# Performance work log

Hardware: AMD Instinct MI355X
Metric: run time of the kernel (lower is better)

## Reference

```python
import jax, jax.numpy as jnp
import numpy as np

B, T, I, H = 4096, 128, 32, 64


def _u(key, shape, bound):
    return jax.random.uniform(key, shape, jnp.float32, -bound, bound)


def setup_inputs() -> dict:
    key = jax.random.key(0)
    ks = jax.random.split(key, 14)
    bound = 1.0 / np.sqrt(H)  # torch LSTM/Linear default init scale
    inp = {
        "x": jax.random.normal(ks[0], (B, T, I), jnp.float32),
        "Wih0": _u(ks[1], (4 * H, I), bound),
        "Whh0": _u(ks[2], (4 * H, H), bound),
        "bih0": _u(ks[3], (4 * H,), bound),
        "bhh0": _u(ks[4], (4 * H,), bound),
        "Wih1": _u(ks[5], (4 * H, H), bound),
        "Whh1": _u(ks[6], (4 * H, H), bound),
        "bih1": _u(ks[7], (4 * H,), bound),
        "bhh1": _u(ks[8], (4 * H,), bound),
        "Wc1": _u(ks[9], (32, H), 1.0 / np.sqrt(H)),
        "bc1": _u(ks[10], (32,), 1.0 / np.sqrt(H)),
        "Wc2": _u(ks[11], (1, 32), 1.0 / np.sqrt(32)),
        "bc2": _u(ks[12], (1,), 1.0 / np.sqrt(32)),
    }
    return inp


def lstm_layer(x_tbi, Wih, Whh, bih, bhh):
    """x_tbi: [T, B, in]. Returns (all hidden [T,B,H], final hidden [B,H]).
    PyTorch gate order: i, f, g, o."""
    b = x_tbi.shape[1]
    h0 = jnp.zeros((b, Whh.shape[1]), x_tbi.dtype)
    c0 = jnp.zeros_like(h0)
    # precompute input projections for all timesteps in one big GEMM
    xproj = jnp.einsum('tbi,gi->tbg', x_tbi, Wih) + (bih + bhh)

    def step(carry, xp_t):
        h, c = carry
        gates = xp_t + h @ Whh.T  # [B, 4H]
        i, f, g, o = jnp.split(gates, 4, axis=-1)
        c = jax.nn.sigmoid(f) * c + jax.nn.sigmoid(i) * jnp.tanh(g)
        h = jax.nn.sigmoid(o) * jnp.tanh(c)
        return (h, c), h

    (hT, _), hs = jax.lax.scan(step, (h0, c0), xproj)
    return hs, hT


def reference(x, Wih0, Whh0, bih0, bhh0, Wih1, Whh1, bih1, bhh1, Wc1, bc1, Wc2, bc2):
    x_tbi = jnp.transpose(x, (1, 0, 2))  # [T, B, I]
    hs0, _ = lstm_layer(x_tbi, Wih0, Whh0, bih0, bhh0)
    # dropout between layers is identity in eval mode
    _, hT = lstm_layer(hs0, Wih1, Whh1, bih1, bhh1)  # h_n[-1]: [B, H]
    hidden = jax.nn.relu(hT @ Wc1.T + bc1)  # [B, 32]; classifier dropout = identity (eval)
    out = hidden @ Wc2.T + bc2  # [B, 1]
    return out.squeeze(-1)  # [B]
```

## Files before the change

kernel.cpp:

```cpp
#include <hip/hip_runtime.h>


#define TT 128
#define II 32
#define HH 64

typedef _Float16 half8 __attribute__((ext_vector_type(8)));
typedef float floatx4 __attribute__((ext_vector_type(4)));

#define LOG2E 1.4426950408889634f

__device__ __forceinline__ half8 load_w_frag(const float* __restrict__ W, int n, int K, int k0) {
    const float* p = W + (size_t)n * K + k0;
    float4 a = *(const float4*)p;
    float4 b = *(const float4*)(p + 4);
    half8 h;
    h[0] = (_Float16)a.x; h[1] = (_Float16)a.y; h[2] = (_Float16)a.z; h[3] = (_Float16)a.w;
    h[4] = (_Float16)b.x; h[5] = (_Float16)b.y; h[6] = (_Float16)b.z; h[7] = (_Float16)b.w;
    return h;
}

__device__ __forceinline__ float sig_tanh(float a, float b) {
    float bb = fminf(fmaxf(b, -15.f), 15.f);
    float u  = __builtin_amdgcn_exp2f(bb * (2.0f * LOG2E));
    float v  = __builtin_amdgcn_exp2f(-a * LOG2E);
    float num = u - 1.0f;
    float d1  = u + 1.0f;
    float den = fmaf(v, d1, d1);
    return num * __builtin_amdgcn_rcpf(den);
}

__device__ __forceinline__ float fsig(float x) {
    return __builtin_amdgcn_rcpf(1.0f + __builtin_amdgcn_exp2f(-x * LOG2E));
}

__global__ __launch_bounds__(512, 2) void lstm_fused(
    const float* __restrict__ x,
    const float* __restrict__ Wih0, const float* __restrict__ Whh0,
    const float* __restrict__ bih0, const float* __restrict__ bhh0,
    const float* __restrict__ Wih1, const float* __restrict__ Whh1,
    const float* __restrict__ bih1, const float* __restrict__ bhh1,
    const float* __restrict__ Wc1, const float* __restrict__ bc1,
    const float* __restrict__ Wc2, const float* __restrict__ bc2,
    float* __restrict__ out)
{
    __shared__ __align__(16) _Float16 xs[2][16][40];
    __shared__ __align__(16) _Float16 h0s[2][16][72];
    __shared__ __align__(16) _Float16 h1s[2][16][72];
    __shared__ __align__(16) float h1f[16][68];
    __shared__ float hid[16][32];

    const int tid  = threadIdx.x;
    const int wid  = tid >> 6;
    const int w4   = wid & 3;
    const bool isL0 = (wid < 4);
    const int lane = tid & 63;
    const int q  = lane >> 4;
    const int lr = lane & 15;
    const int b0 = blockIdx.x * 16;

    half8 bx0[4], bh0[4][2];
    half8 bi1[4][2], bh1[4][2];
    float biasv[4];
    if (isL0) {
        #pragma unroll
        for (int g = 0; g < 4; ++g) {
            int n = (w4 + 4 * g) * 16 + lr;
            bx0[g]    = load_w_frag(Wih0, n, 32, q * 8);
            bh0[g][0] = load_w_frag(Whh0, n, 64, q * 8);
            bh0[g][1] = load_w_frag(Whh0, n, 64, 32 + q * 8);
            biasv[g]  = bih0[n] + bhh0[n];
        }
    } else {
        #pragma unroll
        for (int g = 0; g < 4; ++g) {
            int n = (w4 + 4 * g) * 16 + lr;
            bi1[g][0] = load_w_frag(Wih1, n, 64, q * 8);
            bi1[g][1] = load_w_frag(Wih1, n, 64, 32 + q * 8);
            bh1[g][0] = load_w_frag(Whh1, n, 64, q * 8);
            bh1[g][1] = load_w_frag(Whh1, n, 64, 32 + q * 8);
            biasv[g]  = bih1[n] + bhh1[n];
        }
    }

    for (int i = tid; i < 2 * 16 * 72; i += 512) {
        ((_Float16*)h0s)[i] = (_Float16)0.0f;
        ((_Float16*)h1s)[i] = (_Float16)0.0f;
    }

    float cr[4] = {0.f, 0.f, 0.f, 0.f};

    const int xm = (tid >> 4) & 15;
    const int xf = (tid & 15) * 2;
    const float* xrow = x + ((size_t)(b0 + xm) * TT) * II + xf;
    float2 xbuf = {0.f, 0.f};
    if (isL0) {
        float2 x0 = *(const float2*)(xrow);
        xs[0][xm][xf]     = (_Float16)x0.x;
        xs[0][xm][xf + 1] = (_Float16)x0.y;
        if (TT > 1) xbuf = *(const float2*)(xrow + 1 * II);
    }

    for (int k = 0; k <= TT; ++k) {
        __syncthreads();

        const int rd = (k + 1) & 1;
        const int wr = k & 1;
        const bool doL0 = isL0 && (k < TT);
        const bool doL1 = (!isL0) && (k >= 1);
        float hnew[4];
        float2 xnew = xbuf;

        if (doL0) {
            half8 xfrag = *(const half8*)&xs[wr][lr][q * 8];
            half8 h0a   = *(const half8*)&h0s[rd][lr][q * 8];
            half8 h0b   = *(const half8*)&h0s[rd][lr][32 + q * 8];
            if (k + 2 < TT) xnew = *(const float2*)(xrow + (size_t)(k + 2) * II);
            floatx4 a0[4];
            #pragma unroll
            for (int g = 0; g < 4; ++g) {
                floatx4 acc = {biasv[g], biasv[g], biasv[g], biasv[g]};
                acc = __builtin_amdgcn_mfma_f32_16x16x32_f16(xfrag, bx0[g],    acc, 0, 0, 0);
                acc = __builtin_amdgcn_mfma_f32_16x16x32_f16(h0a,   bh0[g][0], acc, 0, 0, 0);
                acc = __builtin_amdgcn_mfma_f32_16x16x32_f16(h0b,   bh0[g][1], acc, 0, 0, 0);
                a0[g] = acc;
            }
            #pragma unroll
            for (int r = 0; r < 4; ++r) {
                float sf = fsig(a0[1][r]);
                float c  = fmaf(sf, cr[r], sig_tanh(a0[0][r], a0[2][r]));
                cr[r] = c;
                hnew[r] = sig_tanh(a0[3][r], c);
            }
        }
        if (doL1) {
            half8 g0a = *(const half8*)&h0s[rd][lr][q * 8];
            half8 g0b = *(const half8*)&h0s[rd][lr][32 + q * 8];
            half8 h1a = *(const half8*)&h1s[rd][lr][q * 8];
            half8 h1b = *(const half8*)&h1s[rd][lr][32 + q * 8];
            floatx4 a1[4];
            #pragma unroll
            for (int g = 0; g < 4; ++g) {
                floatx4 acc = {biasv[g], biasv[g], biasv[g], biasv[g]};
                acc = __builtin_amdgcn_mfma_f32_16x16x32_f16(g0a, bi1[g][0], acc, 0, 0, 0);
                acc = __builtin_amdgcn_mfma_f32_16x16x32_f16(g0b, bi1[g][1], acc, 0, 0, 0);
                acc = __builtin_amdgcn_mfma_f32_16x16x32_f16(h1a, bh1[g][0], acc, 0, 0, 0);
                acc = __builtin_amdgcn_mfma_f32_16x16x32_f16(h1b, bh1[g][1], acc, 0, 0, 0);
                a1[g] = acc;
            }
            #pragma unroll
            for (int r = 0; r < 4; ++r) {
                float sf = fsig(a1[1][r]);
                float c  = fmaf(sf, cr[r], sig_tanh(a1[0][r], a1[2][r]));
                cr[r] = c;
                hnew[r] = sig_tanh(a1[3][r], c);
            }
        }

        if (doL0) {
            #pragma unroll
            for (int r = 0; r < 4; ++r)
                h0s[wr][q * 4 + r][w4 * 16 + lr] = (_Float16)hnew[r];
            if (k + 1 < TT) {
                xs[rd][xm][xf]     = (_Float16)xbuf.x;
                xs[rd][xm][xf + 1] = (_Float16)xbuf.y;
            }
            xbuf = xnew;
        }
        if (doL1) {
            if (k == TT) {
                #pragma unroll
                for (int r = 0; r < 4; ++r)
                    h1f[q * 4 + r][w4 * 16 + lr] = hnew[r];
            } else {
                #pragma unroll
                for (int r = 0; r < 4; ++r)
                    h1s[wr][q * 4 + r][w4 * 16 + lr] = (_Float16)hnew[r];
            }
        }
    }
    __syncthreads();

    if (tid < 256) {
        int m = tid >> 4;
        int u = (tid & 15) * 2;
        float a = bc1[u], b = bc1[u + 1];
        const float* w0 = Wc1 + u * 64;
        const float* w1 = Wc1 + (u + 1) * 64;
        #pragma unroll 8
        for (int kk = 0; kk < 64; ++kk) {
            float hv = h1f[m][kk];
            a += hv * w0[kk];
            b += hv * w1[kk];
        }
        hid[m][u]     = fmaxf(a, 0.f);
        hid[m][u + 1] = fmaxf(b, 0.f);
    }
    __syncthreads();
    if (tid < 16) {
        float o = bc2[0];
        #pragma unroll
        for (int u = 0; u < 32; ++u) o += hid[tid][u] * Wc2[u];
        out[b0 + tid] = o;
    }
}

extern "C" void kernel_launch(void* const* d_in, const int* in_sizes, int n_in,
                              void* d_out, int out_size, void* d_ws, size_t ws_size,
                              hipStream_t stream) {
    (void)in_sizes; (void)n_in; (void)d_ws; (void)ws_size; (void)out_size;
    const float* x    = (const float*)d_in[0];
    const float* Wih0 = (const float*)d_in[1];
    const float* Whh0 = (const float*)d_in[2];
    const float* bih0 = (const float*)d_in[3];
    const float* bhh0 = (const float*)d_in[4];
    const float* Wih1 = (const float*)d_in[5];
    const float* Whh1 = (const float*)d_in[6];
    const float* bih1 = (const float*)d_in[7];
    const float* bhh1 = (const float*)d_in[8];
    const float* Wc1  = (const float*)d_in[9];
    const float* bc1  = (const float*)d_in[10];
    const float* Wc2  = (const float*)d_in[11];
    const float* bc2  = (const float*)d_in[12];
    lstm_fused<<<dim3(256), dim3(512), 0, stream>>>(
        x, Wih0, Whh0, bih0, bhh0, Wih1, Whh1, bih1, bhh1, Wc1, bc1, Wc2, bc2,
        (float*)d_out);
}
```

Baseline: 203.5 us.

## Precompute next-step input projection off critical path and fold bias into activations

After: 255.8 us. 25.7% more time.

```diff
diff --git a/kernel.cpp b/kernel.cpp
--- a/kernel.cpp
+++ b/kernel.cpp
@@ -3,35 +3,22 @@
 
 #define TT 128
 #define II 32
-#define HH 64
 
 typedef _Float16 half8 __attribute__((ext_vector_type(8)));
 typedef float floatx4 __attribute__((ext_vector_type(4)));
 
 #define LOG2E 1.4426950408889634f
 
-__device__ __forceinline__ half8 load_w_frag(const float* __restrict__ W, int n, int K, int k0) {
-    const float* p = W + (size_t)n * K + k0;
-    float4 a = *(const float4*)p;
-    float4 b = *(const float4*)(p + 4);
+__device__ __forceinline__ half8 cvt_frag(float4 a, float4 b) {
     half8 h;
     h[0] = (_Float16)a.x; h[1] = (_Float16)a.y; h[2] = (_Float16)a.z; h[3] = (_Float16)a.w;
     h[4] = (_Float16)b.x; h[5] = (_Float16)b.y; h[6] = (_Float16)b.z; h[7] = (_Float16)b.w;
     return h;
 }
 
-__device__ __forceinline__ float sig_tanh(float a, float b) {
-    float bb = fminf(fmaxf(b, -15.f), 15.f);
-    float u  = __builtin_amdgcn_exp2f(bb * (2.0f * LOG2E));
-    float v  = __builtin_amdgcn_exp2f(-a * LOG2E);
-    float num = u - 1.0f;
-    float d1  = u + 1.0f;
-    float den = fmaf(v, d1, d1);
-    return num * __builtin_amdgcn_rcpf(den);
-}
-
-__device__ __forceinline__ float fsig(float x) {
-    return __builtin_amdgcn_rcpf(1.0f + __builtin_amdgcn_exp2f(-x * LOG2E));
+__device__ __forceinline__ half8 load_w_frag(const float* __restrict__ W, int n, int K, int k0) {
+    const float* p = W + (size_t)n * K + k0;
+    return cvt_frag(*(const float4*)p, *(const float4*)(p + 4));
 }
 
 __global__ __launch_bounds__(512, 2) void lstm_fused(
@@ -44,7 +31,6 @@
     const float* __restrict__ Wc2, const float* __restrict__ bc2,
     float* __restrict__ out)
 {
-    __shared__ __align__(16) _Float16 xs[2][16][40];
     __shared__ __align__(16) _Float16 h0s[2][16][72];
     __shared__ __align__(16) _Float16 h1s[2][16][72];
     __shared__ __align__(16) float h1f[16][68];
@@ -59,9 +45,13 @@
     const int lr = lane & 15;
     const int b0 = blockIdx.x * 16;
 
+    const float nL  = -LOG2E;
+    const float p2L = 2.0f * LOG2E;
+    const float C43 = 30.0f * LOG2E;
+
     half8 bx0[4], bh0[4][2];
     half8 bi1[4][2], bh1[4][2];
-    float biasv[4];
+    float bias[4];
     if (isL0) {
         #pragma unroll
         for (int g = 0; g < 4; ++g) {
@@ -69,7 +59,7 @@
             bx0[g]    = load_w_frag(Wih0, n, 32, q * 8);
             bh0[g][0] = load_w_frag(Whh0, n, 64, q * 8);
             bh0[g][1] = load_w_frag(Whh0, n, 64, 32 + q * 8);
-            biasv[g]  = bih0[n] + bhh0[n];
+            bias[g]   = bih0[n] + bhh0[n];
         }
     } else {
         #pragma unroll
@@ -79,8 +69,24 @@
             bi1[g][1] = load_w_frag(Wih1, n, 64, 32 + q * 8);
             bh1[g][0] = load_w_frag(Whh1, n, 64, q * 8);
             bh1[g][1] = load_w_frag(Whh1, n, 64, 32 + q * 8);
-            biasv[g]  = bih1[n] + bhh1[n];
-        }
+            bias[g]   = bih1[n] + bhh1[n];
+        }
+    }
+    const float nbi = nL * bias[0], nbf = nL * bias[1];
+    const float bg2 = p2L * bias[2], nbo = nL * bias[3];
+
+    const floatx4 zeroq = {0.f, 0.f, 0.f, 0.f};
+
+    const float* xlane = x + (size_t)(b0 + lr) * TT * II + q * 8;
+    float4 xr0, xr1;
+    floatx4 xacc[4];
+    if (isL0) {
+        half8 xf = cvt_frag(*(const float4*)xlane, *(const float4*)(xlane + 4));
+        #pragma unroll
+        for (int g = 0; g < 4; ++g)
+            xacc[g] = __builtin_amdgcn_mfma_f32_16x16x32_f16(xf, bx0[g], zeroq, 0, 0, 0);
+        xr0 = *(const float4*)(xlane + II);
+        xr1 = *(const float4*)(xlane + II + 4);
     }
 
     for (int i = tid; i < 2 * 16 * 72; i += 512) {
@@ -89,17 +95,6 @@
     }
 
     float cr[4] = {0.f, 0.f, 0.f, 0.f};
-
-    const int xm = (tid >> 4) & 15;
-    const int xf = (tid & 15) * 2;
-    const float* xrow = x + ((size_t)(b0 + xm) * TT) * II + xf;
-    float2 xbuf = {0.f, 0.f};
-    if (isL0) {
-        float2 x0 = *(const float2*)(xrow);
-        xs[0][xm][xf]     = (_Float16)x0.x;
-        xs[0][xm][xf + 1] = (_Float16)x0.y;
-        if (TT > 1) xbuf = *(const float2*)(xrow + 1 * II);
-    }
 
     for (int k = 0; k <= TT; ++k) {
         __syncthreads();
@@ -108,29 +103,16 @@
         const int wr = k & 1;
         const bool doL0 = isL0 && (k < TT);
         const bool doL1 = (!isL0) && (k >= 1);
+        floatx4 a[4];
         float hnew[4];
-        float2 xnew = xbuf;
 
         if (doL0) {
-            half8 xfrag = *(const half8*)&xs[wr][lr][q * 8];
-            half8 h0a   = *(const half8*)&h0s[rd][lr][q * 8];
-            half8 h0b   = *(const half8*)&h0s[rd][lr][32 + q * 8];
-            if (k + 2 < TT) xnew = *(const float2*)(xrow + (size_t)(k + 2) * II);
-            floatx4 a0[4];
+            half8 h0a = *(const half8*)&h0s[rd][lr][q * 8];
+            half8 h0b = *(const half8*)&h0s[rd][lr][32 + q * 8];
             #pragma unroll
             for (int g = 0; g < 4; ++g) {
-                floatx4 acc = {biasv[g], biasv[g], biasv[g], biasv[g]};
-                acc = __builtin_amdgcn_mfma_f32_16x16x32_f16(xfrag, bx0[g],    acc, 0, 0, 0);
-                acc = __builtin_amdgcn_mfma_f32_16x16x32_f16(h0a,   bh0[g][0], acc, 0, 0, 0);
-                acc = __builtin_amdgcn_mfma_f32_16x16x32_f16(h0b,   bh0[g][1], acc, 0, 0, 0);
-                a0[g] = acc;
-            }
-            #pragma unroll
-            for (int r = 0; r < 4; ++r) {
-                float sf = fsig(a0[1][r]);
-                float c  = fmaf(sf, cr[r], sig_tanh(a0[0][r], a0[2][r]));
-                cr[r] = c;
-                hnew[r] = sig_tanh(a0[3][r], c);
+                floatx4 t = __builtin_amdgcn_mfma_f32_16x16x32_f16(h0a, bh0[g][0], xacc[g], 0, 0, 0);
+                a[g]      = __builtin_amdgcn_mfma_f32_16x16x32_f16(h0b, bh0[g][1], t,       0, 0, 0);
             }
         }
         if (doL1) {
@@ -138,22 +120,31 @@
             half8 g0b = *(const half8*)&h0s[rd][lr][32 + q * 8];
             half8 h1a = *(const half8*)&h1s[rd][lr][q * 8];
             half8 h1b = *(const half8*)&h1s[rd][lr][32 + q * 8];
-            floatx4 a1[4];
             #pragma unroll
             for (int g = 0; g < 4; ++g) {
-                floatx4 acc = {biasv[g], biasv[g], biasv[g], biasv[g]};
-                acc = __builtin_amdgcn_mfma_f32_16x16x32_f16(g0a, bi1[g][0], acc, 0, 0, 0);
-                acc = __builtin_amdgcn_mfma_f32_16x16x32_f16(g0b, bi1[g][1], acc, 0, 0, 0);
-                acc = __builtin_amdgcn_mfma_f32_16x16x32_f16(h1a, bh1[g][0], acc, 0, 0, 0);
-                acc = __builtin_amdgcn_mfma_f32_16x16x32_f16(h1b, bh1[g][1], acc, 0, 0, 0);
-                a1[g] = acc;
-            }
+                floatx4 t = __builtin_amdgcn_mfma_f32_16x16x32_f16(g0a, bi1[g][0], zeroq, 0, 0, 0);
+                t         = __builtin_amdgcn_mfma_f32_16x16x32_f16(g0b, bi1[g][1], t,     0, 0, 0);
+                t         = __builtin_amdgcn_mfma_f32_16x16x32_f16(h1a, bh1[g][0], t,     0, 0, 0);
+                a[g]      = __builtin_amdgcn_mfma_f32_16x16x32_f16(h1b, bh1[g][1], t,     0, 0, 0);
+            }
+        }
+        if (doL0 || doL1) {
             #pragma unroll
             for (int r = 0; r < 4; ++r) {
-                float sf = fsig(a1[1][r]);
-                float c  = fmaf(sf, cr[r], sig_tanh(a1[0][r], a1[2][r]));
+                float vf = __builtin_amdgcn_exp2f(fmaf(a[1][r], nL, nbf));
+                float sf = __builtin_amdgcn_rcpf(1.0f + vf);
+                float tg = __builtin_amdgcn_fmed3f(fmaf(a[2][r], p2L, bg2), -C43, C43);
+                float u  = __builtin_amdgcn_exp2f(tg);
+                float vi = __builtin_amdgcn_exp2f(fmaf(a[0][r], nL, nbi));
+                float d1 = u + 1.0f;
+                float st = (u - 1.0f) * __builtin_amdgcn_rcpf(fmaf(vi, d1, d1));
+                float c  = fmaf(sf, cr[r], st);
                 cr[r] = c;
-                hnew[r] = sig_tanh(a1[3][r], c);
+                float vo = __builtin_amdgcn_exp2f(fmaf(a[3][r], nL, nbo));
+                float tc = __builtin_amdgcn_fmed3f(c * p2L, -C43, C43);
+                float uc = __builtin_amdgcn_exp2f(tc);
+                float dc = uc + 1.0f;
+                hnew[r] = (uc - 1.0f) * __builtin_amdgcn_rcpf(fmaf(vo, dc, dc));
             }
         }
 
@@ -162,10 +153,15 @@
             for (int r = 0; r < 4; ++r)
                 h0s[wr][q * 4 + r][w4 * 16 + lr] = (_Float16)hnew[r];
             if (k + 1 < TT) {
-                xs[rd][xm][xf]     = (_Float16)xbuf.x;
-                xs[rd][xm][xf + 1] = (_Float16)xbuf.y;
-            }
-            xbuf = xnew;
+                half8 xf = cvt_frag(xr0, xr1);
+                if (k + 2 < TT) {
+                    xr0 = *(const float4*)(xlane + (size_t)(k + 2) * II);
+                    xr1 = *(const float4*)(xlane + (size_t)(k + 2) * II + 4);
+                }
+                #pragma unroll
+                for (int g = 0; g < 4; ++g)
+                    xacc[g] = __builtin_amdgcn_mfma_f32_16x16x32_f16(xf, bx0[g], zeroq, 0, 0, 0);
+            }
         }
         if (doL1) {
             if (k == TT) {
@@ -184,17 +180,17 @@
     if (tid < 256) {
         int m = tid >> 4;
         int u = (tid & 15) * 2;
-        float a = bc1[u], b = bc1[u + 1];
+        float aa = bc1[u], bb = bc1[u + 1];
         const float* w0 = Wc1 + u * 64;
         const float* w1 = Wc1 + (u + 1) * 64;
         #pragma unroll 8
         for (int kk = 0; kk < 64; ++kk) {
             float hv = h1f[m][kk];
-            a += hv * w0[kk];
-            b += hv * w1[kk];
-        }
-        hid[m][u]     = fmaxf(a, 0.f);
-        hid[m][u + 1] = fmaxf(b, 0.f);
+            aa += hv * w0[kk];
+            bb += hv * w1[kk];
+        }
+        hid[m][u]     = fmaxf(aa, 0.f);
+        hid[m][u + 1] = fmaxf(bb, 0.f);
     }
     __syncthreads();
     if (tid < 16) {
```
